# Kernel tuning notes

Hardware: AMD Instinct MI355X
Metric: run time of the kernel (lower is better)

## Reference

```python
import jax, jax.numpy as jnp
import numpy as np

NEG = jnp.float32(-1e9)


def setup_inputs() -> dict:
    key = jax.random.key(0)
    ks = jax.random.split(key, 8)
    B, S, D = 8, 2048, 1024
    scale = 1.0 / np.sqrt(D)
    return {
        "xQ": jax.random.normal(ks[0], (B, S, D), jnp.float32),
        "xK": jax.random.normal(ks[1], (B, S, D), jnp.float32),
        "xV": jax.random.normal(ks[2], (B, S, D), jnp.float32),
        "padding_mask": jax.random.randint(ks[3], (B, S), 0, 2, jnp.int32),
        "casual_mask": jnp.ones((B, S), jnp.int32),
        "W_q": jax.random.normal(ks[4], (D, D), jnp.float32) * scale,
        "b_q": jnp.zeros((D,), jnp.float32),
        "W_k": jax.random.normal(ks[5], (D, D), jnp.float32) * scale,
        "b_k": jnp.zeros((D,), jnp.float32),
        "W_v": jax.random.normal(ks[6], (D, D), jnp.float32) * scale,
        "b_v": jnp.zeros((D,), jnp.float32),
    }


def reference(xQ, xK, xV, padding_mask, casual_mask, W_q, b_q, W_k, b_k, W_v, b_v):
    # Linear projections (torch nn.Linear: x @ W.T + b)
    Q = jnp.einsum('bsd,ed->bse', xQ, W_q) + b_q
    K = jnp.einsum('bsd,ed->bse', xK, W_k) + b_k
    V = jnp.einsum('bsd,ed->bse', xV, W_v) + b_v

    # Raw logits (note: original code applies NO 1/sqrt(dk) scaling)
    QKT = jnp.einsum('bqd,bkd->bqk', Q, K)  # [B, Sq, Sk]

    # Additive padding mask: -1e9 on padded key positions
    pad = jnp.where(padding_mask[:, None, :] == 0, NEG, jnp.float32(0.0))
    # Additive causal mask: -1e9 above the diagonal
    Sq, Sk = QKT.shape[1], QKT.shape[2]
    caus = jnp.where(
        jnp.tril(jnp.ones((Sq, Sk), dtype=bool)), jnp.float32(0.0), NEG
    )[None, :, :]
    QKT = QKT + pad + caus

    S = jax.nn.softmax(QKT, axis=-1)
    return jnp.einsum('bqk,bkd->bqd', S, V)
```

## Files before the change

### kernel.cpp

```cpp
#include <hip/hip_runtime.h>

typedef __attribute__((ext_vector_type(4))) float f4;
typedef __attribute__((ext_vector_type(4))) float f32x4;
typedef _Float16 half4 __attribute__((ext_vector_type(4)));
typedef _Float16 half8 __attribute__((ext_vector_type(8)));

#define DEVI static __device__ __forceinline__

DEVI void gload_lds16(const void* g, void* l) {
  __builtin_amdgcn_global_load_lds(
      (const __attribute__((address_space(1))) void*)g,
      (__attribute__((address_space(3))) void*)l, 16, 0, 0);
}

#define PIPE_SYNC(N)                                     \
  asm volatile("s_waitcnt vmcnt(" #N ")" ::: "memory");  \
  __builtin_amdgcn_sched_barrier(0);                     \
  __builtin_amdgcn_s_barrier();                          \
  __builtin_amdgcn_sched_barrier(0);

template <int SL>
__global__ __launch_bounds__(256) void cvt_split(const float* __restrict__ X,
                                                 _Float16* __restrict__ H,
                                                 _Float16* __restrict__ L,
                                                 int n4) {
  int i = blockIdx.x * 256 + threadIdx.x;
  const int stride = gridDim.x * 256;
  for (; i < n4; i += stride) {
    f4 x = ((const f4*)X)[i];
    half4 h, l;
#pragma unroll
    for (int j = 0; j < 4; ++j) {
      h[j] = (_Float16)x[j];
      if (SL) l[j] = (_Float16)(x[j] - (float)h[j]);
    }
    ((half4*)H)[i] = h;
    if (SL) ((half4*)L)[i] = l;
  }
}

template <int SPLIT>
DEVI void gemm_core(const _Float16* __restrict__ A0,
                    const _Float16* __restrict__ A1,
                    const _Float16* __restrict__ B0, int lda, int ldb, int NS,
                    _Float16* lds, f32x4 (&acc)[8][4]) {
  const int tid = threadIdx.x;
  const int w = tid >> 6, lane = tid & 63;
  const int wm = w >> 2, wn = w & 3;
  const int r16 = lane & 15, kg = lane >> 4;
  _Float16* LA = lds;
  _Float16* LB = lds + 4 * 256 * 32;

  auto STAGE = [&](int t) {
    const int kc = SPLIT ? (t >> 1) : t;
    const _Float16* As = (SPLIT && (t & 1)) ? A1 : A0;
    const _Float16* ab = As + kc * 32;
    const _Float16* bb = B0 + kc * 32;
    _Float16* la = LA + (t & 3) * (256 * 32);
    _Float16* lb = LB + (t & 3) * (256 * 32);
#pragma unroll
    for (int j = 0; j < 2; ++j) {
      int g = j * 512 + w * 64 + lane;
      int row = g >> 2, c = g & 3;
      int cs = (c ^ (row >> 1)) & 3;
      gload_lds16(ab + (size_t)row * lda + cs * 8,
                  la + ((size_t)j * 512 + w * 64) * 8);
      gload_lds16(bb + (size_t)row * ldb + cs * 8,
                  lb + ((size_t)j * 512 + w * 64) * 8);
    }
  };

  auto COMPUTE = [&](int t) {
    const _Float16* la = LA + (t & 3) * (256 * 32);
    const _Float16* lb = LB + (t & 3) * (256 * 32);
    half8 af[8], bf[4];
#pragma unroll
    for (int mi = 0; mi < 8; ++mi) {
      int row = wm * 128 + mi * 16 + r16;
      af[mi] = *(const half8*)(la + row * 32 + (((kg ^ (row >> 1)) & 3) * 8));
    }
#pragma unroll
    for (int ni = 0; ni < 4; ++ni) {
      int row = wn * 64 + ni * 16 + r16;
      bf[ni] = *(const half8*)(lb + row * 32 + (((kg ^ (row >> 1)) & 3) * 8));
    }
    __builtin_amdgcn_s_setprio(1);
#pragma unroll
    for (int mi = 0; mi < 8; ++mi)
#pragma unroll
      for (int ni = 0; ni < 4; ++ni)
        acc[mi][ni] = __builtin_amdgcn_mfma_f32_16x16x32_f16(
            af[mi], bf[ni], acc[mi][ni], 0, 0, 0);
    __builtin_amdgcn_s_setprio(0);
  };

  STAGE(0);
  STAGE(1);
  STAGE(2);
  PIPE_SYNC(8);
  int t = 0;
  for (; t < NS - 3; ++t) {
    STAGE(t + 3);
    COMPUTE(t);
    PIPE_SYNC(8);
  }
  COMPUTE(t);
  PIPE_SYNC(4);
  ++t;
  COMPUTE(t);
  PIPE_SYNC(0);
  ++t;
  COMPUTE(t);
}

DEVI void acc_zero(f32x4 (&acc)[8][4]) {
#pragma unroll
  for (int i = 0; i < 8; ++i)
#pragma unroll
    for (int j = 0; j < 4; ++j) acc[i][j] = (f32x4)0.0f;
}

template <int STORE_LO>
__global__ __launch_bounds__(512, 2) void proj_eng_split(
    const _Float16* __restrict__ Xh, const _Float16* __restrict__ Xl,
    const _Float16* __restrict__ Wh, const float* __restrict__ bias,
    _Float16* __restrict__ OutHi, _Float16* __restrict__ OutLo) {
  extern __shared__ _Float16 lds[];
  const int m0 = blockIdx.y * 256, n0 = blockIdx.x * 256;
  f32x4 acc[8][4];
  acc_zero(acc);
  gemm_core<1>(Xh + (size_t)m0 * 1024, Xl + (size_t)m0 * 1024,
               Wh + (size_t)n0 * 1024, 1024, 1024, 64, lds, acc);
  const int tid = threadIdx.x;
  const int w = tid >> 6, lane = tid & 63;
  const int wm = w >> 2, wn = w & 3;
  const int r16 = lane & 15, kg = lane >> 4;
  float bcol[4];
#pragma unroll
  for (int ni = 0; ni < 4; ++ni) bcol[ni] = bias[n0 + wn * 64 + ni * 16 + r16];
#pragma unroll
  for (int mi = 0; mi < 8; ++mi) {
    int row = m0 + wm * 128 + mi * 16 + kg * 4;
#pragma unroll
    for (int ni = 0; ni < 4; ++ni) {
      int col = n0 + wn * 64 + ni * 16 + r16;
#pragma unroll
      for (int j = 0; j < 4; ++j) {
        float v = acc[mi][ni][j] + bcol[ni];
        _Float16 h = (_Float16)v;
        OutHi[(size_t)(row + j) * 1024 + col] = h;
        if (STORE_LO)
          OutLo[(size_t)(row + j) * 1024 + col] = (_Float16)(v - (float)h);
      }
    }
  }
}

__global__ __launch_bounds__(512, 2) void proj_eng_v(
    const _Float16* __restrict__ Xh, const _Float16* __restrict__ Wh,
    const float* __restrict__ bias, _Float16* __restrict__ Vt) {
  extern __shared__ _Float16 lds[];
  const int m0 = blockIdx.y * 256, n0 = blockIdx.x * 256;
  f32x4 acc[8][4];
  acc_zero(acc);
  gemm_core<0>(Xh + (size_t)m0 * 1024, Xh, Wh + (size_t)n0 * 1024, 1024, 1024,
               32, lds, acc);
  const int tid = threadIdx.x;
  const int w = tid >> 6, lane = tid & 63;
  const int wm = w >> 2, wn = w & 3;
  const int r16 = lane & 15, kg = lane >> 4;
  float bcol[4];
#pragma unroll
  for (int ni = 0; ni < 4; ++ni) bcol[ni] = bias[n0 + wn * 64 + ni * 16 + r16];
  __syncthreads();
  _Float16(*T)[256] = (_Float16(*)[256])lds;
#pragma unroll
  for (int mi = 0; mi < 8; ++mi) {
    int ml = wm * 128 + mi * 16 + kg * 4;
#pragma unroll
    for (int ni = 0; ni < 4; ++ni) {
      int nl = wn * 64 + ni * 16 + r16;
#pragma unroll
      for (int j = 0; j < 4; ++j)
        T[nl][ml + j] = (_Float16)(acc[mi][ni][j] + bcol[ni]);
    }
  }
  __syncthreads();
  const int b = m0 >> 11;
  const int s0 = m0 & 2047;
#pragma unroll
  for (int r = 0; r < 16; ++r) {
    int flat = tid + r * 512;
    int n = flat >> 5, c = flat & 31;
    half8 v = *(const half8*)&T[n][c * 8];
    *(half8*)(Vt + (size_t)b * (1024 * 2048) + (size_t)(n0 + n) * 2048 + s0 +
              c * 8) = v;
  }
}

__global__ __launch_bounds__(512, 2) void qk_eng(
    const _Float16* __restrict__ Qh, const _Float16* __restrict__ Ql,
    const _Float16* __restrict__ Kh, float* __restrict__ Lg, int bbase) {
  extern __shared__ _Float16 lds[];
  int t = blockIdx.x;
  int qt = 0, base = 0;
  while (t >= base + qt + 1) { base += qt + 1; ++qt; }
  const int kt = t - base;
  const int y = blockIdx.y;
  const int b = bbase + y;
  const size_t boff = (size_t)b * (2048 * 1024);
  f32x4 acc[8][4];
  acc_zero(acc);
  gemm_core<1>(Qh + boff + (size_t)(qt * 256) * 1024,
               Ql + boff + (size_t)(qt * 256) * 1024,
               Kh + boff + (size_t)(kt * 256) * 1024, 1024, 1024, 64, lds, acc);
  const int tid = threadIdx.x;
  const int w = tid >> 6, lane = tid & 63;
  const int wm = w >> 2, wn = w & 3;
  const int r16 = lane & 15, kg = lane >> 4;
  float* L = Lg + (size_t)y * (2048 * 2048);
#pragma unroll
  for (int mi = 0; mi < 8; ++mi) {
    int row = qt * 256 + wm * 128 + mi * 16 + kg * 4;
#pragma unroll
    for (int ni = 0; ni < 4; ++ni) {
      int col = kt * 256 + wn * 64 + ni * 16 + r16;
#pragma unroll
      for (int j = 0; j < 4; ++j)
        L[(size_t)(row + j) * 2048 + col] = acc[mi][ni][j];
    }
  }
}

__global__ __launch_bounds__(512, 2) void pv_eng(
    const float* __restrict__ Lg, const _Float16* __restrict__ Vt,
    float* __restrict__ Out, int bbase) {
  extern __shared__ _Float16 lds[];
  const int nt = blockIdx.x, qt = blockIdx.y, y = blockIdx.z;
  const int b = bbase + y;
  const _Float16* P = (const _Float16*)(Lg + (size_t)y * (2048 * 2048));
  f32x4 acc[8][4];
  acc_zero(acc);
  gemm_core<0>(P + (size_t)(qt * 256) * 4096, P,
               Vt + (size_t)b * (1024 * 2048) + (size_t)(nt * 256) * 2048, 4096,
               2048, (qt + 1) * 8, lds, acc);
  const int tid = threadIdx.x;
  const int w = tid >> 6, lane = tid & 63;
  const int wm = w >> 2, wn = w & 3;
  const int r16 = lane & 15, kg = lane >> 4;
#pragma unroll
  for (int mi = 0; mi < 8; ++mi) {
    int row = qt * 256 + wm * 128 + mi * 16 + kg * 4;
#pragma unroll
    for (int ni = 0; ni < 4; ++ni) {
      int col = nt * 256 + wn * 64 + ni * 16 + r16;
#pragma unroll
      for (int j = 0; j < 4; ++j)
        Out[(size_t)(b * 2048 + row + j) * 1024 + col] = acc[mi][ni][j];
    }
  }
}

template <int NSPLIT, int STORE_LO>
__global__ __launch_bounds__(256) void proj_kernel(
    const float* __restrict__ X, const float* __restrict__ W,
    const float* __restrict__ bias, _Float16* __restrict__ OutHi,
    _Float16* __restrict__ OutLo) {
  __shared__ struct {
    float As[128][36];
    float Bs[128][36];
  } u;
  const int tid = threadIdx.x;
  const int lane = tid & 63, w = tid >> 6;
  const int wm = w >> 1, wn = w & 1;
  const int r16 = lane & 15, kg = lane >> 4;
  const int m0 = blockIdx.y * 128, n0 = blockIdx.x * 128;
  f32x4 acc[4][4];
#pragma unroll
  for (int i = 0; i < 4; ++i)
#pragma unroll
    for (int j = 0; j < 4; ++j) acc[i][j] = (f32x4)0.0f;
  f4 ra[4], rb[4];
  auto LOAD = [&](int kt) {
#pragma unroll
    for (int r = 0; r < 4; ++r) {
      int flat = tid + r * 256;
      int row = flat >> 3, c = flat & 7;
      ra[r] = *(const f4*)(X + (size_t)(m0 + row) * 1024 + kt * 32 + c * 4);
      rb[r] = *(const f4*)(W + (size_t)(n0 + row) * 1024 + kt * 32 + c * 4);
    }
  };
  LOAD(0);
  for (int kt = 0; kt < 32; ++kt) {
    __syncthreads();
#pragma unroll
    for (int r = 0; r < 4; ++r) {
      int flat = tid + r * 256;
      int row = flat >> 3, c = flat & 7;
      *(f4*)&u.As[row][c * 4] = ra[r];
      *(f4*)&u.Bs[row][c * 4] = rb[r];
    }
    __syncthreads();
    if (kt + 1 < 32) LOAD(kt + 1);
    half8 ah[4], al[4], bh[4];
#pragma unroll
    for (int mi = 0; mi < 4; ++mi) {
      const float* p = &u.As[wm * 64 + mi * 16 + r16][kg * 8];
      f4 x0 = *(const f4*)p, x1 = *(const f4*)(p + 4);
      half8 h, l;
#pragma unroll
      for (int j = 0; j < 4; ++j) {
        h[j] = (_Float16)x0[j];
        h[j + 4] = (_Float16)x1[j];
      }
      ah[mi] = h;
      if (NSPLIT == 2) {
#pragma unroll
        for (int j = 0; j < 4; ++j) {
          l[j] = (_Float16)(x0[j] - (float)h[j]);
          l[j + 4] = (_Float16)(x1[j] - (float)h[j + 4]);
        }
        al[mi] = l;
      }
    }
#pragma unroll
    for (int ni = 0; ni < 4; ++ni) {
      const float* p = &u.Bs[wn * 64 + ni * 16 + r16][kg * 8];
      f4 x0 = *(const f4*)p, x1 = *(const f4*)(p + 4);
      half8 h;
#pragma unroll
      for (int j = 0; j < 4; ++j) {
        h[j] = (_Float16)x0[j];
        h[j + 4] = (_Float16)x1[j];
      }
      bh[ni] = h;
    }
#pragma unroll
    for (int mi = 0; mi < 4; ++mi)
#pragma unroll
      for (int ni = 0; ni < 4; ++ni) {
        acc[mi][ni] = __builtin_amdgcn_mfma_f32_16x16x32_f16(
            ah[mi], bh[ni], acc[mi][ni], 0, 0, 0);
        if (NSPLIT == 2)
          acc[mi][ni] = __builtin_amdgcn_mfma_f32_16x16x32_f16(
              al[mi], bh[ni], acc[mi][ni], 0, 0, 0);
      }
  }
  float bcol[4];
#pragma unroll
  for (int ni = 0; ni < 4; ++ni) bcol[ni] = bias[n0 + wn * 64 + ni * 16 + r16];
#pragma unroll
  for (int mi = 0; mi < 4; ++mi) {
    int row = m0 + wm * 64 + mi * 16 + kg * 4;
#pragma unroll
    for (int ni = 0; ni < 4; ++ni) {
      int col = n0 + wn * 64 + ni * 16 + r16;
#pragma unroll
      for (int j = 0; j < 4; ++j) {
        float v = acc[mi][ni][j] + bcol[ni];
        _Float16 h = (_Float16)v;
        OutHi[(size_t)(row + j) * 1024 + col] = h;
        if (STORE_LO)
          OutLo[(size_t)(row + j) * 1024 + col] = (_Float16)(v - (float)h);
      }
    }
  }
}

__global__ __launch_bounds__(256) void softmax_kernel(
    float* __restrict__ Lg, const int* __restrict__ pad, int bbase) {
  const int q = blockIdx.x;
  const int y = blockIdx.y;
  const int b = bbase + y;
  const int tid = threadIdx.x;
  float* row = Lg + (size_t)y * (2048 * 2048) + (size_t)q * 2048;
  _Float16* prow = (_Float16*)row;
  const int* pb = pad + (size_t)b * 2048;
  const int kend = ((q >> 8) + 1) << 8;
  float v[8];
  int nv = 0;
  float mx = -3.0e38f;
  for (int k = tid; k <= q; k += 256) {
    float l = row[k];
    if (pb[k] == 0) l += -1.0e9f;
    v[nv++] = l;
    mx = fmaxf(mx, l);
  }
  __shared__ float red[4];
  for (int o = 32; o; o >>= 1) mx = fmaxf(mx, __shfl_xor(mx, o));
  if ((tid & 63) == 0) red[tid >> 6] = mx;
  __syncthreads();
  mx = fmaxf(fmaxf(red[0], red[1]), fmaxf(red[2], red[3]));
  __syncthreads();
  float s = 0.f;
  for (int i = 0; i < nv; ++i) s += expf(v[i] - mx);
  for (int o = 32; o; o >>= 1) s += __shfl_xor(s, o);
  if ((tid & 63) == 0) red[tid >> 6] = s;
  __syncthreads();
  s = red[0] + red[1] + red[2] + red[3];
  const float inv = 1.0f / s;
  int i = 0;
  for (int k = tid; k <= q; k += 256) {
    prow[k] = (_Float16)(expf(v[i] - mx) * inv);
    ++i;
  }
  for (int k = q + 1 + tid; k < kend; k += 256) prow[k] = (_Float16)0.0f;
}

__global__ __launch_bounds__(512) void fix_f(const int* __restrict__ pad,
                                             int* __restrict__ fb) {
  const int b = threadIdx.x >> 6, k = threadIdx.x & 63;
  unsigned long long m = __ballot(pad[b * 2048 + k] != 0);
  if (k == 0) fb[b] = m ? (__ffsll((long long)m) - 1) : 64;
}

__global__ __launch_bounds__(256) void fix_qrow2(
    const float* __restrict__ xQ, const float* __restrict__ Wq,
    const float* __restrict__ bq, const int* __restrict__ fb,
    float* __restrict__ Qrow) {
  const int b = blockIdx.y;
  const int f = fb[b];
  const int tid = threadIdx.x;
  const int e = blockIdx.x * 16 + (tid >> 4);
  const int l16 = tid & 15;
  __shared__ float xq[1024];
  for (int q = 0; q < f; ++q) {
    *(f4*)&xq[tid * 4] = ((const f4*)(xQ + (size_t)(b * 2048 + q) * 1024))[tid];
    __syncthreads();
    float a = 0.f;
#pragma unroll
    for (int it = 0; it < 16; ++it) {
      int d = l16 * 4 + it * 64;
      f4 ww = *(const f4*)(Wq + (size_t)e * 1024 + d);
      a += xq[d] * ww[0] + xq[d + 1] * ww[1] + xq[d + 2] * ww[2] +
           xq[d + 3] * ww[3];
    }
    for (int o = 8; o; o >>= 1) a += __shfl_xor(a, o);
    if (l16 == 0) Qrow[((size_t)b * 64 + q) * 1024 + e] = a + bq[e];
    __syncthreads();
  }
}

__global__ __launch_bounds__(256) void fix_qb0(const float* __restrict__ bk,
                                               const int* __restrict__ fb,
                                               const float* __restrict__ Qrow,
                                               float* __restrict__ qb0) {
  const int q = blockIdx.x, b = blockIdx.y;
  if (q >= fb[b]) return;
  const int tid = threadIdx.x;
  const float* qr = Qrow + ((size_t)b * 64 + q) * 1024;
  float p = 0.f;
  for (int e = tid; e < 1024; e += 256) p += qr[e] * bk[e];
  __shared__ float red[4];
  for (int o = 32; o; o >>= 1) p += __shfl_xor(p, o);
  if ((tid & 63) == 0) red[tid >> 6] = p;
  __syncthreads();
  if (tid == 0) qb0[b * 64 + q] = red[0] + red[1] + red[2] + red[3];
}

__global__ __launch_bounds__(256) void fix_g2(const float* __restrict__ Wk,
                                              const int* __restrict__ fb,
                                              const float* __restrict__ Qrow,
                                              float* __restrict__ Gpart) {
  const int b = blockIdx.y;
  const int f = fb[b];
  const int tid = threadIdx.x;
  const int ddblk = blockIdx.x & 3, es = blockIdx.x >> 2;
  const int dd = ddblk * 256 + tid;
  __shared__ float qc[128];
  for (int q = 0; q < f; ++q) {
    if (tid < 32)
      *(f4*)&qc[tid * 4] =
          ((const f4*)(Qrow + ((size_t)b * 64 + q) * 1024 + es * 128))[tid];
    __syncthreads();
    float g = 0.f;
    for (int e = 0; e < 128; ++e)
      g += qc[e] * Wk[(size_t)(es * 128 + e) * 1024 + dd];
    Gpart[(((size_t)es * 8 + b) * 64 + q) * 1024 + dd] = g;
    __syncthreads();
  }
}

__global__ __launch_bounds__(256) void fix_logit2(
    const float* __restrict__ xK, const int* __restrict__ pad,
    const int* __restrict__ fb, const float* __restrict__ Gpart,
    const float* __restrict__ qb0, float* __restrict__ lrow) {
  const int b = blockIdx.y;
  const int f = fb[b];
  const int tid = threadIdx.x;
  const int k = blockIdx.x * 16 + (tid >> 4);
  const int l16 = tid & 15;
  __shared__ float Gs[1024];
  for (int q = 0; q < f; ++q) {
    f4 s = (f4)0.0f;
#pragma unroll
    for (int es = 0; es < 8; ++es)
      s += ((const f4*)(Gpart + (((size_t)es * 8 + b) * 64 + q) * 1024))[tid];
    *(f4*)&Gs[tid * 4] = s;
    __syncthreads();
    float a = 0.f;
#pragma unroll
    for (int it = 0; it < 16; ++it) {
      int d = l16 * 4 + it * 64;
      f4 x = *(const f4*)(xK + (size_t)(b * 2048 + k) * 1024 + d);
      a += x[0] * Gs[d] + x[1] * Gs[d + 1] + x[2] * Gs[d + 2] +
           x[3] * Gs[d + 3];
    }
    for (int o = 8; o; o >>= 1) a += __shfl_xor(a, o);
    if (l16 == 0) {
      float l = a + qb0[b * 64 + q];
      if (pad[b * 2048 + k] == 0) l += -1.0e9f;
      if (k > q) l += -1.0e9f;
      lrow[((size_t)b * 64 + q) * 2048 + k] = l;
    }
    __syncthreads();
  }
}

__global__ __launch_bounds__(256) void fix_sm(const int* __restrict__ fb,
                                              float* __restrict__ lrow,
                                              float* __restrict__ srow) {
  const int q = blockIdx.x, b = blockIdx.y;
  if (q >= fb[b]) return;
  const int tid = threadIdx.x;
  float* row = lrow + ((size_t)b * 64 + q) * 2048;
  float v[8];
  float mx = -3.0e38f;
#pragma unroll
  for (int i = 0; i < 8; ++i) {
    v[i] = row[tid + i * 256];
    mx = fmaxf(mx, v[i]);
  }
  __shared__ float red[4];
  for (int o = 32; o; o >>= 1) mx = fmaxf(mx, __shfl_xor(mx, o));
  if ((tid & 63) == 0) red[tid >> 6] = mx;
  __syncthreads();
  mx = fmaxf(fmaxf(red[0], red[1]), fmaxf(red[2], red[3]));
  __syncthreads();
  float s = 0.f;
#pragma unroll
  for (int i = 0; i < 8; ++i) {
    v[i] = expf(v[i] - mx);
    s += v[i];
  }
#pragma unroll
  for (int i = 0; i < 8; ++i) row[tid + i * 256] = v[i];
  for (int o = 32; o; o >>= 1) s += __shfl_xor(s, o);
  if ((tid & 63) == 0) red[tid >> 6] = s;
  __syncthreads();
  if (tid == 0) srow[b * 64 + q] = red[0] + red[1] + red[2] + red[3];
}

__global__ __launch_bounds__(256) void fix_pv2(
    const _Float16* __restrict__ Vt, const int* __restrict__ fb,
    const float* __restrict__ lrow, const float* __restrict__ srow,
    float* __restrict__ Out) {
  const int b = blockIdx.y;
  const int f = fb[b];
  const int tid = threadIdx.x;
  const int d = blockIdx.x * 16 + (tid >> 4);
  const int l16 = tid & 15;
  __shared__ float ps[2048];
  for (int q = 0; q < f; ++q) {
    const f4* src = (const f4*)(lrow + ((size_t)b * 64 + q) * 2048);
    *(f4*)&ps[tid * 8] = src[tid * 2];
    *(f4*)&ps[tid * 8 + 4] = src[tid * 2 + 1];
    __syncthreads();
    float o = 0.f;
#pragma unroll
    for (int it = 0; it < 16; ++it) {
      int k = l16 * 8 + it * 128;
      half8 vv = *(const half8*)(Vt + (size_t)b * (1024 * 2048) +
                                 (size_t)d * 2048 + k);
      o += (float)vv[0] * ps[k] + (float)vv[1] * ps[k + 1] +
           (float)vv[2] * ps[k + 2] + (float)vv[3] * ps[k + 3] +
           (float)vv[4] * ps[k + 4] + (float)vv[5] * ps[k + 5] +
           (float)vv[6] * ps[k + 6] + (float)vv[7] * ps[k + 7];
    }
    for (int of = 8; of; of >>= 1) o += __shfl_xor(o, of);
    if (l16 == 0)
      Out[(size_t)(b * 2048 + q) * 1024 + d] = o * (1.0f / srow[b * 64 + q]);
    __syncthreads();
  }
}

extern "C" void kernel_launch(void* const* d_in, const int* in_sizes, int n_in,
                              void* d_out, int out_size, void* d_ws,
                              size_t ws_size, hipStream_t stream) {
  const float* xQ = (const float*)d_in[0];
  const float* xK = (const float*)d_in[1];
  const float* xV = (const float*)d_in[2];
  const int* pad = (const int*)d_in[3];
  const float* Wq = (const float*)d_in[5];
  const float* bq = (const float*)d_in[6];
  const float* Wk = (const float*)d_in[7];
  const float* bk = (const float*)d_in[8];
  const float* Wv = (const float*)d_in[9];
  const float* bv = (const float*)d_in[10];
  float* Out = (float*)d_out;

  const size_t MB = (size_t)1 << 20;
  char* wsb = (char*)d_ws;
  _Float16* Qh = (_Float16*)(wsb);
  _Float16* Ql = (_Float16*)(wsb + 32 * MB);
  _Float16* Kh = (_Float16*)(wsb + 64 * MB);
  _Float16* Vt = (_Float16*)(wsb + 96 * MB);
  float* Lg = (float*)(wsb + 128 * MB);

  size_t avail = (ws_size > 128 * MB) ? ws_size - 128 * MB : 0;
  int G = (int)(avail / (16 * MB));
  if (G > 8) G = 8;
  if (G < 1) G = 1;

  const int SMEM = 131072;
  (void)hipFuncSetAttribute((const void*)&proj_eng_split<1>,
                            hipFuncAttributeMaxDynamicSharedMemorySize, SMEM);
  (void)hipFuncSetAttribute((const void*)&proj_eng_split<0>,
                            hipFuncAttributeMaxDynamicSharedMemorySize, SMEM);
  (void)hipFuncSetAttribute((const void*)&proj_eng_v,
                            hipFuncAttributeMaxDynamicSharedMemorySize, SMEM);
  (void)hipFuncSetAttribute((const void*)&qk_eng,
                            hipFuncAttributeMaxDynamicSharedMemorySize, SMEM);
  (void)hipFuncSetAttribute((const void*)&pv_eng,
                            hipFuncAttributeMaxDynamicSharedMemorySize, SMEM);

  dim3 blk(256), eblk(512);

  {
    _Float16* sXh = (_Float16*)(wsb);
    _Float16* sWh = (_Float16*)(wsb + 32 * MB);
    cvt_split<0><<<dim3(2048), blk, 0, stream>>>(xV, sXh, nullptr, 4194304);
    cvt_split<0><<<dim3(1024), blk, 0, stream>>>(Wv, sWh, nullptr, 262144);
    proj_eng_v<<<dim3(4, 64), eblk, SMEM, stream>>>(sXh, sWh, bv, Vt);
  }
  {
    _Float16* sXh = (_Float16*)(wsb);
    _Float16* sXl = (_Float16*)(wsb + 32 * MB);
    _Float16* sWh = (_Float16*)(wsb + 128 * MB);
    cvt_split<1><<<dim3(2048), blk, 0, stream>>>(xK, sXh, sXl, 4194304);
    cvt_split<0><<<dim3(1024), blk, 0, stream>>>(Wk, sWh, nullptr, 262144);
    proj_eng_split<0><<<dim3(4, 64), eblk, SMEM, stream>>>(sXh, sXl, sWh, bk,
                                                           Kh, nullptr);
  }
  if (ws_size >= 195 * MB) {
    _Float16* sXh = (_Float16*)(wsb + 128 * MB);
    _Float16* sXl = (_Float16*)(wsb + 160 * MB);
    _Float16* sWh = (_Float16*)(wsb + 192 * MB);
    cvt_split<1><<<dim3(2048), blk, 0, stream>>>(xQ, sXh, sXl, 4194304);
    cvt_split<0><<<dim3(1024), blk, 0, stream>>>(Wq, sWh, nullptr, 262144);
    proj_eng_split<1><<<dim3(4, 64), eblk, SMEM, stream>>>(sXh, sXl, sWh, bq,
                                                           Qh, Ql);
  } else {
    proj_kernel<2, 1><<<dim3(8, 128), blk, 0, stream>>>(xQ, Wq, bq, Qh, Ql);
  }

  for (int bbase = 0; bbase < 8; bbase += G) {
    int nb = (8 - bbase < G) ? (8 - bbase) : G;
    qk_eng<<<dim3(36, nb), eblk, SMEM, stream>>>(Qh, Ql, Kh, Lg, bbase);
    softmax_kernel<<<dim3(2048, nb), blk, 0, stream>>>(Lg, pad, bbase);
    pv_eng<<<dim3(4, 8, nb), eblk, SMEM, stream>>>(Lg, Vt, Out, bbase);
  }

  int* fb = (int*)(wsb);
  float* qb0 = (float*)(wsb + 4 * 1024);
  float* srow = (float*)(wsb + 8 * 1024);
  float* Qrow = (float*)(wsb + 1 * MB);
  float* Gpart = (float*)(wsb + 4 * MB);
  float* lrow = (float*)(wsb + 20 * MB);

  fix_f<<<dim3(1), dim3(512), 0, stream>>>(pad, fb);
  fix_qrow2<<<dim3(64, 8), blk, 0, stream>>>(xQ, Wq, bq, fb, Qrow);
  fix_qb0<<<dim3(64, 8), blk, 0, stream>>>(bk, fb, Qrow, qb0);
  fix_g2<<<dim3(32, 8), blk, 0, stream>>>(Wk, fb, Qrow, Gpart);
  fix_logit2<<<dim3(128, 8), blk, 0, stream>>>(xK, pad, fb, Gpart, qb0, lrow);
  fix_sm<<<dim3(64, 8), blk, 0, stream>>>(fb, lrow, srow);
  fix_pv2<<<dim3(64, 8), blk, 0, stream>>>(Vt, fb, lrow, srow, Out);
}
```

Before: 581.3 us.

## Shrink GEMM tiles, double-buffer pipeline, split weights instead of activations, XCD swizzle

Replaces the 256x256 four-stage GEMM core with a templated core using smaller tiles (256x128 or 128x256), a two-stage double-buffered pipeline, and lower LDS use, so four blocks can be resident per CU instead of two. The projections now split the weight into hi/lo halves instead of splitting the activations, which keeps the extra-precision term while making one conversion pass smaller. All engine kernels are launched on a 1D grid with an XCD-aware block index swizzle to improve L2 locality. The shallower pipeline and smaller tiles lower per-block data reuse and expose more load latency, in exchange for more occupancy and finer causal-tile granularity.

```diff
diff --git a/kernel.cpp b/kernel.cpp
--- a/kernel.cpp
+++ b/kernel.cpp
@@ -13,11 +13,17 @@
       (__attribute__((address_space(3))) void*)l, 16, 0, 0);
 }
 
-#define PIPE_SYNC(N)                                     \
-  asm volatile("s_waitcnt vmcnt(" #N ")" ::: "memory");  \
-  __builtin_amdgcn_sched_barrier(0);                     \
-  __builtin_amdgcn_s_barrier();                          \
+#define STEP_SYNC()                                     \
+  asm volatile("s_waitcnt vmcnt(0)" ::: "memory");      \
+  __builtin_amdgcn_sched_barrier(0);                    \
+  __builtin_amdgcn_s_barrier();                         \
   __builtin_amdgcn_sched_barrier(0);
+
+DEVI int xcd_swz(int id, int n) {
+  int q = n >> 3, r = n & 7;
+  int x = id & 7, c = id >> 3;
+  return (x < r ? x * (q + 1) : r * (q + 1) + (x - r) * q) + c;
+}
 
 template <int SL>
 __global__ __launch_bounds__(256) void cvt_split(const float* __restrict__ X,
@@ -39,108 +45,119 @@
   }
 }
 
-template <int SPLIT>
-DEVI void gemm_core(const _Float16* __restrict__ A0,
-                    const _Float16* __restrict__ A1,
-                    const _Float16* __restrict__ B0, int lda, int ldb, int NS,
-                    _Float16* lds, f32x4 (&acc)[8][4]) {
+template <int AR, int BR, int ASPLIT, int BSPLIT>
+DEVI void core(const _Float16* __restrict__ A0, const _Float16* __restrict__ A1,
+               const _Float16* __restrict__ B0, const _Float16* __restrict__ B1,
+               int lda, int ldb, int NS, _Float16* lds, f32x4 (&acc)[4][4]) {
+  constexpr int WN = BR / 64;
+  constexpr int ACH = AR * 32;
+  constexpr int BCH = BR * 32;
+  constexpr int CHUNK = ACH * (1 + ASPLIT) + BCH * (1 + BSPLIT);
   const int tid = threadIdx.x;
   const int w = tid >> 6, lane = tid & 63;
-  const int wm = w >> 2, wn = w & 3;
+  const int wm = w / WN, wn = w % WN;
   const int r16 = lane & 15, kg = lane >> 4;
-  _Float16* LA = lds;
-  _Float16* LB = lds + 4 * 256 * 32;
 
   auto STAGE = [&](int t) {
-    const int kc = SPLIT ? (t >> 1) : t;
-    const _Float16* As = (SPLIT && (t & 1)) ? A1 : A0;
-    const _Float16* ab = As + kc * 32;
-    const _Float16* bb = B0 + kc * 32;
-    _Float16* la = LA + (t & 3) * (256 * 32);
-    _Float16* lb = LB + (t & 3) * (256 * 32);
-#pragma unroll
-    for (int j = 0; j < 2; ++j) {
-      int g = j * 512 + w * 64 + lane;
+    _Float16* base = lds + (size_t)(t & 1) * CHUNK;
+#pragma unroll
+    for (int j = 0; j < AR / 128; ++j) {
+      int g = j * 512 + tid;
       int row = g >> 2, c = g & 3;
       int cs = (c ^ (row >> 1)) & 3;
-      gload_lds16(ab + (size_t)row * lda + cs * 8,
-                  la + ((size_t)j * 512 + w * 64) * 8);
-      gload_lds16(bb + (size_t)row * ldb + cs * 8,
-                  lb + ((size_t)j * 512 + w * 64) * 8);
+      size_t src = (size_t)row * lda + cs * 8 + t * 32;
+      int dst = (j * 512 + w * 64) * 8;
+      gload_lds16(A0 + src, base + dst);
+      if (ASPLIT) gload_lds16(A1 + src, base + ACH + dst);
+    }
+    _Float16* bb = base + ACH * (1 + ASPLIT);
+#pragma unroll
+    for (int j = 0; j < BR / 128; ++j) {
+      int g = j * 512 + tid;
+      int row = g >> 2, c = g & 3;
+      int cs = (c ^ (row >> 1)) & 3;
+      size_t src = (size_t)row * ldb + cs * 8 + t * 32;
+      int dst = (j * 512 + w * 64) * 8;
+      gload_lds16(B0 + src, bb + dst);
+      if (BSPLIT) gload_lds16(B1 + src, bb + BCH + dst);
     }
   };
 
   auto COMPUTE = [&](int t) {
-    const _Float16* la = LA + (t & 3) * (256 * 32);
-    const _Float16* lb = LB + (t & 3) * (256 * 32);
-    half8 af[8], bf[4];
-#pragma unroll
-    for (int mi = 0; mi < 8; ++mi) {
-      int row = wm * 128 + mi * 16 + r16;
-      af[mi] = *(const half8*)(la + row * 32 + (((kg ^ (row >> 1)) & 3) * 8));
+    const _Float16* base = lds + (size_t)(t & 1) * CHUNK;
+    const _Float16* la = base;
+    const _Float16* lb = base + ACH * (1 + ASPLIT);
+    half8 a0[4], a1[4], b0[4], b1[4];
+#pragma unroll
+    for (int mi = 0; mi < 4; ++mi) {
+      int row = wm * 64 + mi * 16 + r16;
+      int off = row * 32 + (((kg ^ (row >> 1)) & 3) * 8);
+      a0[mi] = *(const half8*)(la + off);
+      if (ASPLIT) a1[mi] = *(const half8*)(la + ACH + off);
     }
 #pragma unroll
     for (int ni = 0; ni < 4; ++ni) {
       int row = wn * 64 + ni * 16 + r16;
-      bf[ni] = *(const half8*)(lb + row * 32 + (((kg ^ (row >> 1)) & 3) * 8));
+      int off = row * 32 + (((kg ^ (row >> 1)) & 3) * 8);
+      b0[ni] = *(const half8*)(lb + off);
+      if (BSPLIT) b1[ni] = *(const half8*)(lb + BCH + off);
     }
     __builtin_amdgcn_s_setprio(1);
 #pragma unroll
-    for (int mi = 0; mi < 8; ++mi)
-#pragma unroll
-      for (int ni = 0; ni < 4; ++ni)
+    for (int mi = 0; mi < 4; ++mi)
+#pragma unroll
+      for (int ni = 0; ni < 4; ++ni) {
         acc[mi][ni] = __builtin_amdgcn_mfma_f32_16x16x32_f16(
-            af[mi], bf[ni], acc[mi][ni], 0, 0, 0);
+            a0[mi], b0[ni], acc[mi][ni], 0, 0, 0);
+        if (ASPLIT)
+          acc[mi][ni] = __builtin_amdgcn_mfma_f32_16x16x32_f16(
+              a1[mi], b0[ni], acc[mi][ni], 0, 0, 0);
+        if (BSPLIT)
+          acc[mi][ni] = __builtin_amdgcn_mfma_f32_16x16x32_f16(
+              a0[mi], b1[ni], acc[mi][ni], 0, 0, 0);
+      }
     __builtin_amdgcn_s_setprio(0);
   };
 
   STAGE(0);
-  STAGE(1);
-  STAGE(2);
-  PIPE_SYNC(8);
-  int t = 0;
-  for (; t < NS - 3; ++t) {
-    STAGE(t + 3);
+  STEP_SYNC();
+  for (int t = 0; t < NS; ++t) {
+    if (t + 1 < NS) STAGE(t + 1);
     COMPUTE(t);
-    PIPE_SYNC(8);
-  }
-  COMPUTE(t);
-  PIPE_SYNC(4);
-  ++t;
-  COMPUTE(t);
-  PIPE_SYNC(0);
-  ++t;
-  COMPUTE(t);
-}
-
-DEVI void acc_zero(f32x4 (&acc)[8][4]) {
-#pragma unroll
-  for (int i = 0; i < 8; ++i)
+    STEP_SYNC();
+  }
+}
+
+DEVI void acc_zero(f32x4 (&acc)[4][4]) {
+#pragma unroll
+  for (int i = 0; i < 4; ++i)
 #pragma unroll
     for (int j = 0; j < 4; ++j) acc[i][j] = (f32x4)0.0f;
 }
 
 template <int STORE_LO>
-__global__ __launch_bounds__(512, 2) void proj_eng_split(
-    const _Float16* __restrict__ Xh, const _Float16* __restrict__ Xl,
-    const _Float16* __restrict__ Wh, const float* __restrict__ bias,
+__global__ __launch_bounds__(512, 4) void proj_eng(
+    const _Float16* __restrict__ X, const _Float16* __restrict__ Wh,
+    const _Float16* __restrict__ Wl, const float* __restrict__ bias,
     _Float16* __restrict__ OutHi, _Float16* __restrict__ OutLo) {
   extern __shared__ _Float16 lds[];
-  const int m0 = blockIdx.y * 256, n0 = blockIdx.x * 256;
-  f32x4 acc[8][4];
+  const int id = xcd_swz(blockIdx.x, gridDim.x);
+  const int m0 = (id >> 3) * 256, n0 = (id & 7) * 128;
+  f32x4 acc[4][4];
   acc_zero(acc);
-  gemm_core<1>(Xh + (size_t)m0 * 1024, Xl + (size_t)m0 * 1024,
-               Wh + (size_t)n0 * 1024, 1024, 1024, 64, lds, acc);
+  core<256, 128, 0, 1>(X + (size_t)m0 * 1024, nullptr,
+                       Wh + (size_t)n0 * 1024, Wl + (size_t)n0 * 1024, 1024,
+                       1024, 32, lds, acc);
   const int tid = threadIdx.x;
   const int w = tid >> 6, lane = tid & 63;
-  const int wm = w >> 2, wn = w & 3;
+  const int wm = w >> 1, wn = w & 1;
   const int r16 = lane & 15, kg = lane >> 4;
   float bcol[4];
 #pragma unroll
   for (int ni = 0; ni < 4; ++ni) bcol[ni] = bias[n0 + wn * 64 + ni * 16 + r16];
 #pragma unroll
-  for (int mi = 0; mi < 8; ++mi) {
-    int row = m0 + wm * 128 + mi * 16 + kg * 4;
+  for (int mi = 0; mi < 4; ++mi) {
+    int row = m0 + wm * 64 + mi * 16 + kg * 4;
 #pragma unroll
     for (int ni = 0; ni < 4; ++ni) {
       int col = n0 + wn * 64 + ni * 16 + r16;
@@ -156,18 +173,20 @@
   }
 }
 
-__global__ __launch_bounds__(512, 2) void proj_eng_v(
-    const _Float16* __restrict__ Xh, const _Float16* __restrict__ Wh,
+__global__ __launch_bounds__(512, 4) void proj_eng_v(
+    const _Float16* __restrict__ X, const _Float16* __restrict__ Wh,
     const float* __restrict__ bias, _Float16* __restrict__ Vt) {
   extern __shared__ _Float16 lds[];
-  const int m0 = blockIdx.y * 256, n0 = blockIdx.x * 256;
-  f32x4 acc[8][4];
+  const int id = xcd_swz(blockIdx.x, gridDim.x);
+  const int m0 = (id >> 3) * 256, n0 = (id & 7) * 128;
+  f32x4 acc[4][4];
   acc_zero(acc);
-  gemm_core<0>(Xh + (size_t)m0 * 1024, Xh, Wh + (size_t)n0 * 1024, 1024, 1024,
-               32, lds, acc);
+  core<256, 128, 0, 0>(X + (size_t)m0 * 1024, nullptr,
+                       Wh + (size_t)n0 * 1024, nullptr, 1024, 1024, 32, lds,
+                       acc);
   const int tid = threadIdx.x;
   const int w = tid >> 6, lane = tid & 63;
-  const int wm = w >> 2, wn = w & 3;
+  const int wm = w >> 1, wn = w & 1;
   const int r16 = lane & 15, kg = lane >> 4;
   float bcol[4];
 #pragma unroll
@@ -175,8 +194,8 @@
   __syncthreads();
   _Float16(*T)[256] = (_Float16(*)[256])lds;
 #pragma unroll
-  for (int mi = 0; mi < 8; ++mi) {
-    int ml = wm * 128 + mi * 16 + kg * 4;
+  for (int mi = 0; mi < 4; ++mi) {
+    int ml = wm * 64 + mi * 16 + kg * 4;
 #pragma unroll
     for (int ni = 0; ni < 4; ++ni) {
       int nl = wn * 64 + ni * 16 + r16;
@@ -189,7 +208,7 @@
   const int b = m0 >> 11;
   const int s0 = m0 & 2047;
 #pragma unroll
-  for (int r = 0; r < 16; ++r) {
+  for (int r = 0; r < 8; ++r) {
     int flat = tid + r * 512;
     int n = flat >> 5, c = flat & 31;
     half8 v = *(const half8*)&T[n][c * 8];
@@ -198,30 +217,32 @@
   }
 }
 
-__global__ __launch_bounds__(512, 2) void qk_eng(
+__global__ __launch_bounds__(512, 4) void qk_eng(
     const _Float16* __restrict__ Qh, const _Float16* __restrict__ Ql,
     const _Float16* __restrict__ Kh, float* __restrict__ Lg, int bbase) {
   extern __shared__ _Float16 lds[];
-  int t = blockIdx.x;
+  const int id = xcd_swz(blockIdx.x, gridDim.x);
+  const int y = id / 72;
+  int t = id % 72;
   int qt = 0, base = 0;
-  while (t >= base + qt + 1) { base += qt + 1; ++qt; }
+  while (t >= base + (qt >> 1) + 1) { base += (qt >> 1) + 1; ++qt; }
   const int kt = t - base;
-  const int y = blockIdx.y;
   const int b = bbase + y;
   const size_t boff = (size_t)b * (2048 * 1024);
-  f32x4 acc[8][4];
+  f32x4 acc[4][4];
   acc_zero(acc);
-  gemm_core<1>(Qh + boff + (size_t)(qt * 256) * 1024,
-               Ql + boff + (size_t)(qt * 256) * 1024,
-               Kh + boff + (size_t)(kt * 256) * 1024, 1024, 1024, 64, lds, acc);
+  core<128, 256, 1, 0>(Qh + boff + (size_t)(qt * 128) * 1024,
+                       Ql + boff + (size_t)(qt * 128) * 1024,
+                       Kh + boff + (size_t)(kt * 256) * 1024, nullptr, 1024,
+                       1024, 32, lds, acc);
   const int tid = threadIdx.x;
   const int w = tid >> 6, lane = tid & 63;
   const int wm = w >> 2, wn = w & 3;
   const int r16 = lane & 15, kg = lane >> 4;
   float* L = Lg + (size_t)y * (2048 * 2048);
 #pragma unroll
-  for (int mi = 0; mi < 8; ++mi) {
-    int row = qt * 256 + wm * 128 + mi * 16 + kg * 4;
+  for (int mi = 0; mi < 4; ++mi) {
+    int row = qt * 128 + wm * 64 + mi * 16 + kg * 4;
 #pragma unroll
     for (int ni = 0; ni < 4; ++ni) {
       int col = kt * 256 + wn * 64 + ni * 16 + r16;
@@ -232,25 +253,27 @@
   }
 }
 
-__global__ __launch_bounds__(512, 2) void pv_eng(
+__global__ __launch_bounds__(512, 4) void pv_eng(
     const float* __restrict__ Lg, const _Float16* __restrict__ Vt,
     float* __restrict__ Out, int bbase) {
   extern __shared__ _Float16 lds[];
-  const int nt = blockIdx.x, qt = blockIdx.y, y = blockIdx.z;
+  const int id = xcd_swz(blockIdx.x, gridDim.x);
+  const int y = id >> 6;
+  const int qt = (id & 63) >> 2, nt = id & 3;
   const int b = bbase + y;
   const _Float16* P = (const _Float16*)(Lg + (size_t)y * (2048 * 2048));
-  f32x4 acc[8][4];
+  f32x4 acc[4][4];
   acc_zero(acc);
-  gemm_core<0>(P + (size_t)(qt * 256) * 4096, P,
-               Vt + (size_t)b * (1024 * 2048) + (size_t)(nt * 256) * 2048, 4096,
-               2048, (qt + 1) * 8, lds, acc);
+  core<128, 256, 0, 0>(P + (size_t)(qt * 128) * 4096, nullptr,
+                       Vt + (size_t)b * (1024 * 2048) + (size_t)(nt * 256) * 2048,
+                       nullptr, 4096, 2048, ((qt >> 1) + 1) * 8, lds, acc);
   const int tid = threadIdx.x;
   const int w = tid >> 6, lane = tid & 63;
   const int wm = w >> 2, wn = w & 3;
   const int r16 = lane & 15, kg = lane >> 4;
 #pragma unroll
-  for (int mi = 0; mi < 8; ++mi) {
-    int row = qt * 256 + wm * 128 + mi * 16 + kg * 4;
+  for (int mi = 0; mi < 4; ++mi) {
+    int row = qt * 128 + wm * 64 + mi * 16 + kg * 4;
 #pragma unroll
     for (int ni = 0; ni < 4; ++ni) {
       int col = nt * 256 + wn * 64 + ni * 16 + r16;
@@ -612,53 +635,52 @@
   if (G > 8) G = 8;
   if (G < 1) G = 1;
 
-  const int SMEM = 131072;
-  (void)hipFuncSetAttribute((const void*)&proj_eng_split<1>,
-                            hipFuncAttributeMaxDynamicSharedMemorySize, SMEM);
-  (void)hipFuncSetAttribute((const void*)&proj_eng_split<0>,
-                            hipFuncAttributeMaxDynamicSharedMemorySize, SMEM);
+  const int SM_PROJ = 65536, SM_V = 65536, SM_QK = 65536, SM_PV = 49152;
+  (void)hipFuncSetAttribute((const void*)&proj_eng<1>,
+                            hipFuncAttributeMaxDynamicSharedMemorySize, SM_PROJ);
+  (void)hipFuncSetAttribute((const void*)&proj_eng<0>,
+                            hipFuncAttributeMaxDynamicSharedMemorySize, SM_PROJ);
   (void)hipFuncSetAttribute((const void*)&proj_eng_v,
-                            hipFuncAttributeMaxDynamicSharedMemorySize, SMEM);
+                            hipFuncAttributeMaxDynamicSharedMemorySize, SM_V);
   (void)hipFuncSetAttribute((const void*)&qk_eng,
-                            hipFuncAttributeMaxDynamicSharedMemorySize, SMEM);
+                            hipFuncAttributeMaxDynamicSharedMemorySize, SM_QK);
   (void)hipFuncSetAttribute((const void*)&pv_eng,
-                            hipFuncAttributeMaxDynamicSharedMemorySize, SMEM);
+                            hipFuncAttributeMaxDynamicSharedMemorySize, SM_PV);
 
   dim3 blk(256), eblk(512);
 
   {
-    _Float16* sXh = (_Float16*)(wsb);
+    _Float16* sX = (_Float16*)(wsb);
+    _Float16* sW = (_Float16*)(wsb + 32 * MB);
+    cvt_split<0><<<dim3(2048), blk, 0, stream>>>(xV, sX, nullptr, 4194304);
+    cvt_split<0><<<dim3(1024), blk, 0, stream>>>(Wv, sW, nullptr, 262144);
+    proj_eng_v<<<dim3(512), eblk, SM_V, stream>>>(sX, sW, bv, Vt);
+  }
+  {
+    _Float16* sX = (_Float16*)(wsb);
     _Float16* sWh = (_Float16*)(wsb + 32 * MB);
-    cvt_split<0><<<dim3(2048), blk, 0, stream>>>(xV, sXh, nullptr, 4194304);
-    cvt_split<0><<<dim3(1024), blk, 0, stream>>>(Wv, sWh, nullptr, 262144);
-    proj_eng_v<<<dim3(4, 64), eblk, SMEM, stream>>>(sXh, sWh, bv, Vt);
-  }
-  {
-    _Float16* sXh = (_Float16*)(wsb);
-    _Float16* sXl = (_Float16*)(wsb + 32 * MB);
-    _Float16* sWh = (_Float16*)(wsb + 128 * MB);
-    cvt_split<1><<<dim3(2048), blk, 0, stream>>>(xK, sXh, sXl, 4194304);
-    cvt_split<0><<<dim3(1024), blk, 0, stream>>>(Wk, sWh, nullptr, 262144);
-    proj_eng_split<0><<<dim3(4, 64), eblk, SMEM, stream>>>(sXh, sXl, sWh, bk,
-                                                           Kh, nullptr);
-  }
-  if (ws_size >= 195 * MB) {
-    _Float16* sXh = (_Float16*)(wsb + 128 * MB);
-    _Float16* sXl = (_Float16*)(wsb + 160 * MB);
-    _Float16* sWh = (_Float16*)(wsb + 192 * MB);
-    cvt_split<1><<<dim3(2048), blk, 0, stream>>>(xQ, sXh, sXl, 4194304);
-    cvt_split<0><<<dim3(1024), blk, 0, stream>>>(Wq, sWh, nullptr, 262144);
-    proj_eng_split<1><<<dim3(4, 64), eblk, SMEM, stream>>>(sXh, sXl, sWh, bq,
-                                                           Qh, Ql);
+    _Float16* sWl = (_Float16*)(wsb + 34 * MB);
+    cvt_split<0><<<dim3(2048), blk, 0, stream>>>(xK, sX, nullptr, 4194304);
+    cvt_split<1><<<dim3(1024), blk, 0, stream>>>(Wk, sWh, sWl, 262144);
+    proj_eng<0><<<dim3(512), eblk, SM_PROJ, stream>>>(sX, sWh, sWl, bk, Kh,
+                                                      nullptr);
+  }
+  if (ws_size >= 166 * MB) {
+    _Float16* sX = (_Float16*)(wsb + 128 * MB);
+    _Float16* sWh = (_Float16*)(wsb + 160 * MB);
+    _Float16* sWl = (_Float16*)(wsb + 162 * MB);
+    cvt_split<0><<<dim3(2048), blk, 0, stream>>>(xQ, sX, nullptr, 4194304);
+    cvt_split<1><<<dim3(1024), blk, 0, stream>>>(Wq, sWh, sWl, 262144);
+    proj_eng<1><<<dim3(512), eblk, SM_PROJ, stream>>>(sX, sWh, sWl, bq, Qh, Ql);
   } else {
     proj_kernel<2, 1><<<dim3(8, 128), blk, 0, stream>>>(xQ, Wq, bq, Qh, Ql);
   }
 
   for (int bbase = 0; bbase < 8; bbase += G) {
     int nb = (8 - bbase < G) ? (8 - bbase) : G;
-    qk_eng<<<dim3(36, nb), eblk, SMEM, stream>>>(Qh, Ql, Kh, Lg, bbase);
+    qk_eng<<<dim3(72 * nb), eblk, SM_QK, stream>>>(Qh, Ql, Kh, Lg, bbase);
     softmax_kernel<<<dim3(2048, nb), blk, 0, stream>>>(Lg, pad, bbase);
-    pv_eng<<<dim3(4, 8, nb), eblk, SMEM, stream>>>(Lg, Vt, Out, bbase);
+    pv_eng<<<dim3(64 * nb), eblk, SM_PV, stream>>>(Lg, Vt, Out, bbase);
   }
 
   int* fb = (int*)(wsb);
```

New measurement: 497.7 us. -14.4%, faster.
